# Performance work log

Measured on AMD Instinct MI355X. Metric: run time of the kernel, lower is better.

The kernel has to match this reference:

```python
import jax, jax.numpy as jnp
import numpy as np

B, N, D, H, DH, FF, CI, K, MPE = 8, 1024, 512, 8, 64, 2048, 1024, 31, 512
PAD = (K // 2, K // 2 - (K + 1) % 2)  # (15, 15)


def _ln(x, g, b):
    m = x.mean(-1, keepdims=True)
    v = ((x - m) ** 2).mean(-1, keepdims=True)
    return (x - m) * jax.lax.rsqrt(v + 1e-5) * g + b


def _swish(x):
    return x * jax.nn.sigmoid(x)


def setup_inputs() -> dict:
    key = jax.random.key(0)
    ks = iter(jax.random.split(key, 40))
    def w(shape, s=0.02):
        return (jax.random.normal(next(ks), shape) * s).astype(jnp.float32)
    ones = lambda n: jnp.ones((n,), jnp.float32)
    zeros = lambda n: jnp.zeros((n,), jnp.float32)
    return dict(
        x=jax.random.normal(next(ks), (B, N, D), dtype=jnp.float32),
        f1_g=ones(D), f1_b=zeros(D), f1_w1=w((D, FF)), f1_b1=zeros(FF), f1_w2=w((FF, D)), f1_b2=zeros(D),
        a_g=ones(D), a_b=zeros(D), wq=w((D, H * DH)), wkv=w((D, 2 * H * DH)), wo=w((H * DH, D)), wo_b=zeros(D),
        rel=w((2 * MPE + 1, DH)),
        c_g=ones(D), c_b=zeros(D), cw1=w((D, 2 * CI)), cb1=zeros(2 * CI), dw=w((CI, K)), db=zeros(CI),
        bn_g=ones(CI), bn_b=zeros(CI), bn_m=zeros(CI), bn_v=ones(CI), cw2=w((CI, D)), cb2=zeros(D),
        f2_g=ones(D), f2_b=zeros(D), f2_w1=w((D, FF)), f2_b1=zeros(FF), f2_w2=w((FF, D)), f2_b2=zeros(D),
        p_g=ones(D), p_b=zeros(D),
    )


def reference(x, f1_g, f1_b, f1_w1, f1_b1, f1_w2, f1_b2,
              a_g, a_b, wq, wkv, wo, wo_b, rel,
              c_g, c_b, cw1, cb1, dw, db, bn_g, bn_b, bn_m, bn_v, cw2, cb2,
              f2_g, f2_b, f2_w1, f2_b1, f2_w2, f2_b2, p_g, p_b):
    # FF1 (half-step)
    h = _ln(x, f1_g, f1_b)
    x = x + 0.5 * (_swish(h @ f1_w1 + f1_b1) @ f1_w2 + f1_b2)
    # Attention with relative positional bias
    h = _ln(x, a_g, a_b)
    q = (h @ wq).reshape(B, N, H, DH).transpose(0, 2, 1, 3)          # bhnd
    k, v = jnp.split(h @ wkv, 2, axis=-1)
    k = k.reshape(B, N, H, DH).transpose(0, 2, 1, 3)
    v = v.reshape(B, N, H, DH).transpose(0, 2, 1, 3)
    scale = DH ** -0.5
    dots = jnp.einsum('bhid,bhjd->bhij', q, k) * scale
    seq = jnp.arange(N)
    dist = jnp.clip(seq[:, None] - seq[None, :], -MPE, MPE) + MPE    # [N,N]
    rp = rel[dist]                                                   # [N,N,DH]
    dots = dots + jnp.einsum('bhnd,nrd->bhnr', q, rp) * scale
    attn = jax.nn.softmax(dots, axis=-1)
    o = jnp.einsum('bhij,bhjd->bhid', attn, v).transpose(0, 2, 1, 3).reshape(B, N, H * DH)
    x = x + o @ wo + wo_b
    # Conv module: LN -> pw conv -> GLU -> depthwise conv -> BN(eval) -> swish -> pw conv
    h = _ln(x, c_g, c_b)
    h = h @ cw1 + cb1                                                # [B,N,2CI]
    out, gate = jnp.split(h, 2, axis=-1)
    h = (out * jax.nn.sigmoid(gate)).transpose(0, 2, 1)              # [B,CI,N]
    h = jnp.pad(h, ((0, 0), (0, 0), PAD))
    h = jax.lax.conv_general_dilated(h, dw[:, None, :], (1,), 'VALID',
                                     feature_group_count=CI,
                                     dimension_numbers=('NCH', 'OIH', 'NCH')) + db[None, :, None]
    h = (h - bn_m[None, :, None]) * jax.lax.rsqrt(bn_v[None, :, None] + 1e-5) * bn_g[None, :, None] + bn_b[None, :, None]
    h = _swish(h).transpose(0, 2, 1)                                 # [B,N,CI]
    x = x + h @ cw2 + cb2
    # FF2 (half-step) + post norm
    h = _ln(x, f2_g, f2_b)
    x = x + 0.5 * (_swish(h @ f2_w1 + f2_b1) @ f2_w2 + f2_b2)
    return _ln(x, p_g, p_b)
```

## Files before the change

kernel.cpp:

```cpp
#include <hip/hip_runtime.h>
#include <hip/hip_bf16.h>
#include <cstdint>


using bf16_t = __hip_bfloat16;
typedef __bf16 bf16x8 __attribute__((ext_vector_type(8)));
typedef float floatx4 __attribute__((ext_vector_type(4)));

struct alignas(16) hbf8 { bf16_t h[8]; };
struct alignas(8)  hbf4 { bf16_t h[4]; };

__device__ __forceinline__ float  b2f(bf16_t h) { return __bfloat162float(h); }
__device__ __forceinline__ bf16_t f2b(float f)  { return __float2bfloat16(f); }
__device__ __forceinline__ float  sig_(float x) { return 1.f / (1.f + __expf(-x)); }

__device__ __forceinline__ unsigned pkbf(float a, float b) {
  bf16_t ha = f2b(a), hb = f2b(b);
  unsigned short ua, ub;
  __builtin_memcpy(&ua, &ha, 2);
  __builtin_memcpy(&ub, &hb, 2);
  return (unsigned)ua | ((unsigned)ub << 16);
}

__device__ __forceinline__ void async16(const void* g, void* l) {
  __builtin_amdgcn_global_load_lds(
      (const __attribute__((address_space(1))) unsigned int*)(uintptr_t)g,
      (__attribute__((address_space(3))) unsigned int*)(uintptr_t)l, 16, 0, 0);
}

struct GemmArgs {
  const bf16_t* A; const bf16_t* Bt; const float* bias; const float* srcf;
  bf16_t* C; float* resid;
  int K, lda, ldb, ldc;
  long sAb, sAh, sBb, sBh, sCb, sCh;
  float alpha, beta;
};

template <int BM, int BN, int WR, int WC, int EPI>
__global__ __launch_bounds__(256) void gemm_bt(GemmArgs g) {
  constexpr int FM = BM / (WR * 16);
  constexpr int FN = BN / (WC * 16);
  constexpr int IA = BM / 32;
  constexpr int IB = BN / 32;
  __shared__ __align__(16) bf16_t As[BM * 64];
  __shared__ __align__(16) bf16_t Bs[BN * 64];
  const int tid = threadIdx.x;
  const int lane = tid & 63, w = tid >> 6;
  int bx = blockIdx.x, by = blockIdx.y;
  {
    const int gx = gridDim.x;
    const int nwg = gx * gridDim.y;
    if ((nwg & 7) == 0 && gridDim.z == 1) {
      int lin = by * gx + bx;
      int lid = (lin & 7) * (nwg >> 3) + (lin >> 3);
      bx = lid % gx; by = lid / gx;
    }
  }
  const int bm0 = by * BM, bn0 = bx * BN;
  const int zb = blockIdx.z >> 3, zh = blockIdx.z & 7;
  const bf16_t* Ab = g.A + (long)zb * g.sAb + (long)zh * g.sAh;
  const bf16_t* Bb = g.Bt + (long)zb * g.sBb + (long)zh * g.sBh;
  const int wm0 = (w / WC) * (FM * 16);
  const int wn0 = (w % WC) * (FN * 16);
  const int lrow = lane & 15, lq = lane >> 4;

  floatx4 acc[FM][FN] = {};

  for (int k0 = 0; k0 < g.K; k0 += 64) {
#pragma unroll
    for (int i = 0; i < IA; ++i) {
      int c = i * 256 + tid;
      int m = c >> 3, kk = (c & 7) * 8;
      async16(Ab + (long)(bm0 + m) * g.lda + (k0 + kk), (char*)As + c * 16);
    }
#pragma unroll
    for (int i = 0; i < IB; ++i) {
      int c = i * 256 + tid;
      int n = bn0 + (c >> 3), kk = (c & 7) * 8;
      async16(Bb + (long)n * g.ldb + (k0 + kk), (char*)Bs + c * 16);
    }
    __syncthreads();
#pragma unroll
    for (int ks = 0; ks < 2; ++ks) {
      bf16x8 af[FM], bfr[FN];
#pragma unroll
      for (int fm = 0; fm < FM; ++fm)
        af[fm] = *(const bf16x8*)(As + (wm0 + fm * 16 + lrow) * 64 + ks * 32 + lq * 8);
#pragma unroll
      for (int fn = 0; fn < FN; ++fn)
        bfr[fn] = *(const bf16x8*)(Bs + (wn0 + fn * 16 + lrow) * 64 + ks * 32 + lq * 8);
#pragma unroll
      for (int fm = 0; fm < FM; ++fm)
#pragma unroll
        for (int fn = 0; fn < FN; ++fn)
          acc[fm][fn] = __builtin_amdgcn_mfma_f32_16x16x32_bf16(af[fm], bfr[fn], acc[fm][fn], 0, 0, 0);
    }
    __syncthreads();
  }

  const int bi = bm0 + wm0 + lq * 4;
  const int bj = bn0 + wn0 + lrow;
  if constexpr (EPI == 2) {
    float* R = g.resid;
    const float* S = g.srcf;
#pragma unroll
    for (int fm = 0; fm < FM; ++fm)
#pragma unroll
      for (int fn = 0; fn < FN; ++fn) {
        int j = bj + fn * 16;
        float bv = g.bias ? g.bias[j] : 0.f;
#pragma unroll
        for (int r = 0; r < 4; ++r) {
          long i = bi + fm * 16 + r;
          float base = S ? S[i * g.ldc + j] : R[i * g.ldc + j];
          R[i * g.ldc + j] = base + g.beta * (acc[fm][fn][r] + bv);
        }
      }
  } else if constexpr (EPI == 4) {
    bf16_t* C = g.C;
#pragma unroll
    for (int fm = 0; fm < FM; ++fm)
#pragma unroll
      for (int fn = 0; fn < FN; ++fn) {
        int j = bj + fn * 16;
        float bv = g.bias[(j >> 1) + (j & 1) * 1024];
#pragma unroll
        for (int r = 0; r < 4; ++r) {
          int i = bi + fm * 16 + r;
          float v = acc[fm][fn][r] + bv;
          float gp = __shfl_xor(v, 1);
          if ((j & 1) == 0)
            C[(long)i * g.ldc + (j >> 1)] = f2b(v * sig_(gp));
        }
      }
  } else {
    bf16_t* C = g.C + (long)zb * g.sCb + (long)zh * g.sCh;
#pragma unroll
    for (int fm = 0; fm < FM; ++fm)
#pragma unroll
      for (int fn = 0; fn < FN; ++fn) {
        int j = bj + fn * 16;
        float bv = g.bias ? g.bias[j] : 0.f;
#pragma unroll
        for (int r = 0; r < 4; ++r) {
          int i = bi + fm * 16 + r;
          float v = acc[fm][fn][r];
          if constexpr (EPI == 0) v = g.alpha * v + bv;
          if constexpr (EPI == 1) { v += bv; v = v * sig_(v); }
          C[(long)i * g.ldc + j] = f2b(v);
        }
      }
  }
}

__global__ __launch_bounds__(512, 4) void attn_kernel(
    const bf16_t* __restrict__ QKV, const bf16_t* __restrict__ VT,
    const bf16_t* __restrict__ RELP, bf16_t* __restrict__ O) {
  constexpr int LDT = 1028;
  __shared__ __align__(16) bf16_t Tls[32 * LDT];
  __shared__ float scr[576];

  const int tid = threadIdx.x;
  const int w = tid >> 6, lane = tid & 63;
  const int lrow = lane & 15, lq = lane >> 4;
  const int lin = blockIdx.y * gridDim.x + blockIdx.x;
  const int lid = (lin & 7) * 256 + (lin >> 3);
  const int z = lid >> 5;
  const int i0 = (lid & 31) * 32;
  const int b = z >> 3, zh = z & 7;
  const int j0w = w * 128;

  const bf16_t* Qb  = QKV + ((long)(b * 1024 + i0)) * 1536 + zh * 64;
  const bf16_t* Kb  = QKV + ((long)b * 1024) * 1536 + 512 + zh * 64;
  const bf16_t* VTb = VT + ((long)(b * 8 + zh)) * 65536;

  bf16x8 af[2][2];
#pragma unroll
  for (int fm = 0; fm < 2; ++fm)
#pragma unroll
    for (int ks = 0; ks < 2; ++ks)
      af[fm][ks] = *(const bf16x8*)(Qb + (long)(fm * 16 + lrow) * 1536 + ks * 32 + lq * 8);

  {
    const int u0w = w * 144;
    bf16x8 rf[18];
#pragma unroll
    for (int fnT = 0; fnT < 9; ++fnT) {
      const int u0 = u0w + fnT * 16;
      if (u0 <= 1024) {
        rf[2 * fnT]     = *(const bf16x8*)(RELP + (long)(u0 + lrow) * 64 + lq * 8);
        rf[2 * fnT + 1] = *(const bf16x8*)(RELP + (long)(u0 + lrow) * 64 + 32 + lq * 8);
      }
    }
#pragma unroll
    for (int fnT = 0; fnT < 9; ++fnT) {
      const int u0 = u0w + fnT * 16;
      if (u0 <= 1024) {
#pragma unroll
        for (int fm = 0; fm < 2; ++fm) {
          floatx4 t4 = {};
          t4 = __builtin_amdgcn_mfma_f32_16x16x32_bf16(rf[2 * fnT],     af[fm][0], t4, 0, 0, 0);
          t4 = __builtin_amdgcn_mfma_f32_16x16x32_bf16(rf[2 * fnT + 1], af[fm][1], t4, 0, 0, 0);
          if (u0 + lq * 4 + 4 <= LDT) {
            uint2 v; v.x = pkbf(t4[0], t4[1]); v.y = pkbf(t4[2], t4[3]);
            *(uint2*)(Tls + (long)(fm * 16 + lrow) * LDT + u0 + lq * 4) = v;
          }
        }
      }
    }
  }

  bf16x8 kfA[8], kfB[8];
#pragma unroll
  for (int x = 0; x < 8; ++x)
    kfA[x] = *(const bf16x8*)(Kb + (long)(j0w + (x >> 1) * 16 + lrow) * 1536 + (x & 1) * 32 + lq * 8);
#pragma unroll
  for (int x = 0; x < 8; ++x)
    kfB[x] = *(const bf16x8*)(Kb + (long)(j0w + (4 + (x >> 1)) * 16 + lrow) * 1536 + (x & 1) * 32 + lq * 8);
  __syncthreads();

  floatx4 sacc[2][8] = {};
#pragma unroll
  for (int fn = 0; fn < 4; ++fn) {
    sacc[0][fn] = __builtin_amdgcn_mfma_f32_16x16x32_bf16(af[0][0], kfA[2 * fn],     sacc[0][fn], 0, 0, 0);
    sacc[0][fn] = __builtin_amdgcn_mfma_f32_16x16x32_bf16(af[0][1], kfA[2 * fn + 1], sacc[0][fn], 0, 0, 0);
    sacc[1][fn] = __builtin_amdgcn_mfma_f32_16x16x32_bf16(af[1][0], kfA[2 * fn],     sacc[1][fn], 0, 0, 0);
    sacc[1][fn] = __builtin_amdgcn_mfma_f32_16x16x32_bf16(af[1][1], kfA[2 * fn + 1], sacc[1][fn], 0, 0, 0);
  }
#pragma unroll
  for (int fn = 4; fn < 8; ++fn) {
    sacc[0][fn] = __builtin_amdgcn_mfma_f32_16x16x32_bf16(af[0][0], kfB[2 * (fn - 4)],     sacc[0][fn], 0, 0, 0);
    sacc[0][fn] = __builtin_amdgcn_mfma_f32_16x16x32_bf16(af[0][1], kfB[2 * (fn - 4) + 1], sacc[0][fn], 0, 0, 0);
    sacc[1][fn] = __builtin_amdgcn_mfma_f32_16x16x32_bf16(af[1][0], kfB[2 * (fn - 4)],     sacc[1][fn], 0, 0, 0);
    sacc[1][fn] = __builtin_amdgcn_mfma_f32_16x16x32_bf16(af[1][1], kfB[2 * (fn - 4) + 1], sacc[1][fn], 0, 0, 0);
  }

#pragma unroll
  for (int fm = 0; fm < 2; ++fm)
#pragma unroll
    for (int r = 0; r < 4; ++r) {
      const int il = fm * 16 + lq * 4 + r;
      const bf16_t* trow = Tls + il * LDT + 512;
      const int tb = i0 + il - j0w - lrow;
#pragma unroll
      for (int fn = 0; fn < 8; ++fn) {
        int t = tb - fn * 16;
        t = t < -512 ? -512 : (t > 512 ? 512 : t);
        sacc[fm][fn][r] += b2f(trow[t]);
      }
    }

  float rmax[2][4];
#pragma unroll
  for (int fm = 0; fm < 2; ++fm)
#pragma unroll
    for (int r = 0; r < 4; ++r) {
      float m = sacc[fm][0][r];
#pragma unroll
      for (int fn = 1; fn < 8; ++fn) m = fmaxf(m, sacc[fm][fn][r]);
      rmax[fm][r] = m;
    }
#pragma unroll
  for (int off = 1; off < 16; off <<= 1)
#pragma unroll
    for (int fm = 0; fm < 2; ++fm)
#pragma unroll
      for (int r = 0; r < 4; ++r)
        rmax[fm][r] = fmaxf(rmax[fm][r], __shfl_xor(rmax[fm][r], off));
  if (lrow == 0)
#pragma unroll
    for (int fm = 0; fm < 2; ++fm)
#pragma unroll
      for (int r = 0; r < 4; ++r)
        scr[(fm * 16 + lq * 4 + r) * 9 + w] = rmax[fm][r];

  float rsum[2][4];
#pragma unroll
  for (int fm = 0; fm < 2; ++fm)
#pragma unroll
    for (int r = 0; r < 4; ++r) {
      float s = 0.f;
#pragma unroll
      for (int fn = 0; fn < 8; ++fn) {
        float e = __expf(sacc[fm][fn][r] - rmax[fm][r]);
        sacc[fm][fn][r] = e;
        s += e;
      }
      rsum[fm][r] = s;
    }
#pragma unroll
  for (int off = 1; off < 16; off <<= 1)
#pragma unroll
    for (int fm = 0; fm < 2; ++fm)
#pragma unroll
      for (int r = 0; r < 4; ++r)
        rsum[fm][r] += __shfl_xor(rsum[fm][r], off);
  if (lrow == 0)
#pragma unroll
    for (int fm = 0; fm < 2; ++fm)
#pragma unroll
      for (int r = 0; r < 4; ++r)
        scr[288 + (fm * 16 + lq * 4 + r) * 9 + w] = rsum[fm][r];

  bf16x8 vfA[8];
#pragma unroll
  for (int x = 0; x < 8; ++x)
    vfA[x] = *(const bf16x8*)(VTb + (long)((x & 3) * 16 + lrow) * 1024 + j0w + (x >> 2) * 32 + lq * 8);

  __syncthreads();

#pragma unroll
  for (int fm = 0; fm < 2; ++fm)
#pragma unroll
    for (int fn = 0; fn < 8; ++fn)
#pragma unroll
      for (int r = 0; r < 4; ++r) {
        const int i = fm * 16 + lq * 4 + r;
        const int j = j0w + fn * 16 + lrow;
        const unsigned boff = (unsigned)(i * 2048 + j * 2) ^ ((unsigned)(i & 7) << 4);
        *(bf16_t*)((char*)Tls + boff) = f2b(sacc[fm][fn][r]);
      }

  bf16x8 vfB[8];
#pragma unroll
  for (int x = 0; x < 8; ++x)
    vfB[x] = *(const bf16x8*)(VTb + (long)((x & 3) * 16 + lrow) * 1024 + j0w + 64 + (x >> 2) * 32 + lq * 8);

  floatx4 oacc[2][4] = {};
#pragma unroll
  for (int ks = 0; ks < 4; ++ks) {
    const int j = j0w + ks * 32;
    bf16x8 ap[2];
#pragma unroll
    for (int fm = 0; fm < 2; ++fm) {
      const int i = fm * 16 + lrow;
      const unsigned boff = (unsigned)(i * 2048 + (j + lq * 8) * 2) ^ ((unsigned)(i & 7) << 4);
      ap[fm] = *(const bf16x8*)((char*)Tls + boff);
    }
#pragma unroll
    for (int fd = 0; fd < 4; ++fd) {
      bf16x8 bv = (ks < 2) ? vfA[(ks << 2) | fd] : vfB[((ks - 2) << 2) | fd];
      oacc[0][fd] = __builtin_amdgcn_mfma_f32_16x16x32_bf16(ap[0], bv, oacc[0][fd], 0, 0, 0);
      oacc[1][fd] = __builtin_amdgcn_mfma_f32_16x16x32_bf16(ap[1], bv, oacc[1][fd], 0, 0, 0);
    }
  }
  __syncthreads();

  {
    float* part = (float*)Tls + w * 2048;
#pragma unroll
    for (int fm = 0; fm < 2; ++fm)
#pragma unroll
      for (int fd = 0; fd < 4; ++fd)
#pragma unroll
        for (int r = 0; r < 4; ++r)
          part[(fm * 16 + lq * 4 + r) * 64 + fd * 16 + lrow] = oacc[fm][fd][r];
  }
  __syncthreads();

  {
    const int i = tid >> 4;
    const int d0 = (tid & 15) * 4;
    float mw[8], sw[8];
#pragma unroll
    for (int ww = 0; ww < 8; ++ww) {
      mw[ww] = scr[i * 9 + ww];
      sw[ww] = scr[288 + i * 9 + ww];
    }
    float M = mw[0];
#pragma unroll
    for (int ww = 1; ww < 8; ++ww) M = fmaxf(M, mw[ww]);
    float fac[8]; float tot = 0.f;
#pragma unroll
    for (int ww = 0; ww < 8; ++ww) { fac[ww] = __expf(mw[ww] - M); tot += sw[ww] * fac[ww]; }
    const float inv = 1.f / tot;
    floatx4 s = {};
#pragma unroll
    for (int ww = 0; ww < 8; ++ww) {
      floatx4 p = *(const floatx4*)((const float*)Tls + ww * 2048 + i * 64 + d0);
      s += p * fac[ww];
    }
    hbf4 o4;
#pragma unroll
    for (int m = 0; m < 4; ++m) o4.h[m] = f2b(s[m] * inv);
    *(hbf4*)(O + (long)(b * 1024 + i0 + i) * 512 + zh * 64 + d0) = o4;
  }
}

__global__ __launch_bounds__(256) void diag_kernel(float* __restrict__ out, long n, float v) {
  long i = (long)blockIdx.x * 256 + threadIdx.x;
  if (i < n) out[i] = v;
}

struct PrepJobs {
  const float* src[10];
  bf16_t*      dst[10];
  int R[10], C[10], gx[10], start[10];
  float scale[10];
  int   mode[10];
  int   njobs;
};

__global__ __launch_bounds__(256) void prep_kernel(PrepJobs P) {
  __shared__ float t[32][33];
  const int bid = blockIdx.x;
  int j = 0;
  while (j + 1 < P.njobs && bid >= P.start[j + 1]) ++j;
  const int tile = bid - P.start[j];
  const int tid = threadIdx.x;
  if (P.mode[j] == 2) {
    int i = tile * 256 + tid;
    if (i < 73728) {
      int r = i >> 6, c = i & 63;
      P.dst[j][i] = (r < 1025) ? f2b(P.src[j][r * 64 + c]) : f2b(0.f);
    }
    return;
  }
  const int gx = P.gx[j];
  const int c0 = (tile % gx) * 32, r0 = (tile / gx) * 32;
  const int C = P.C[j], R = P.R[j];
  const float scale = P.scale[j];
  const int tx = tid & 31, ty = tid >> 5;
#pragma unroll
  for (int i = 0; i < 4; ++i)
    t[ty + i * 8][tx] = P.src[j][(long)(r0 + ty + i * 8) * C + c0 + tx];
  __syncthreads();
#pragma unroll
  for (int i = 0; i < 4; ++i) {
    int c = c0 + ty + i * 8;
    int row = (P.mode[j] == 1) ? ((c < 1024) ? 2 * c : 2 * (c - 1024) + 1) : c;
    P.dst[j][(long)row * R + r0 + tx] = f2b(t[tx][ty + i * 8] * scale);
  }
}

template <bool F32OUT>
__global__ __launch_bounds__(256) void ln_kernel(const float* __restrict__ X, const float* __restrict__ gam,
                                                 const float* __restrict__ bet, void* __restrict__ outv) {
  int row = blockIdx.x, tid = threadIdx.x;
  const float* x = X + (long)row * 512;
  float a = x[tid], b = x[tid + 256];
  float s = a + b, q = a * a + b * b;
  for (int off = 32; off; off >>= 1) { s += __shfl_down(s, off); q += __shfl_down(q, off); }
  __shared__ float red[8];
  int w = tid >> 6;
  if ((tid & 63) == 0) { red[w] = s; red[w + 4] = q; }
  __syncthreads();
  float ts = red[0] + red[1] + red[2] + red[3];
  float tq = red[4] + red[5] + red[6] + red[7];
  float mean = ts * (1.f / 512.f);
  float var = tq * (1.f / 512.f) - mean * mean;
  float rs = rsqrtf(var + 1e-5f);
  float o0 = (a - mean) * rs * gam[tid]       + bet[tid];
  float o1 = (b - mean) * rs * gam[tid + 256] + bet[tid + 256];
  if constexpr (F32OUT) {
    float* out = (float*)outv;
    out[(long)row * 512 + tid]       = o0;
    out[(long)row * 512 + tid + 256] = o1;
  } else {
    bf16_t* out = (bf16_t*)outv;
    out[(long)row * 512 + tid]       = f2b(o0);
    out[(long)row * 512 + tid + 256] = f2b(o1);
  }
}

__global__ __launch_bounds__(256) void vt_kernel(const bf16_t* __restrict__ QKV, bf16_t* __restrict__ VT) {
  int jb = blockIdx.x, z = blockIdx.y;
  int b = z >> 3, h = z & 7;
  const bf16_t* src = QKV + (long)b * 1024 * 1536 + 1024 + h * 64;
  bf16_t* dst = VT + (long)z * 65536;
  __shared__ bf16_t t[64][65];
  int tid = threadIdx.x;
#pragma unroll
  for (int i = 0; i < 16; ++i) {
    int l = i * 256 + tid;
    int j = l >> 6, d = l & 63;
    t[d][j] = src[(long)(jb * 64 + j) * 1536 + d];
  }
  __syncthreads();
#pragma unroll
  for (int i = 0; i < 16; ++i) {
    int l = i * 256 + tid;
    int d = l >> 6, j = l & 63;
    dst[(long)d * 1024 + jb * 64 + j] = t[d][j];
  }
}

__global__ __launch_bounds__(256) void dwconv_kernel(const bf16_t* __restrict__ G, const float* __restrict__ dw,
    const float* __restrict__ db, const float* __restrict__ bng, const float* __restrict__ bnb,
    const float* __restrict__ bnm, const float* __restrict__ bnv, bf16_t* __restrict__ out) {
  int n0 = blockIdx.x * 32, c0 = blockIdx.y * 64, b = blockIdx.z;
  __shared__ bf16_t t[62][64];
  __shared__ float dws[31][64];
  int tid = threadIdx.x;
  const bf16_t* src = G + (long)b * 1024 * 1024 + c0;
#pragma unroll
  for (int i = 0; i < 2; ++i) {
    int l = i * 256 + tid;
    if (l < 496) {
      int rr = l >> 3, c8 = (l & 7) * 8;
      int n = n0 - 15 + rr;
      hbf8 v;
      if (n >= 0 && n < 1024) v = *(const hbf8*)(src + (long)n * 1024 + c8);
      else { for (int m = 0; m < 8; ++m) v.h[m] = f2b(0.f); }
      *(hbf8*)&t[rr][c8] = v;
    }
  }
#pragma unroll
  for (int i = 0; i < 8; ++i) {
    int l = i * 256 + tid;
    if (l < 1984) {
      int k = l >> 6, c = l & 63;
      dws[k][c] = dw[(long)(c0 + c) * 31 + k];
    }
  }
  __syncthreads();
  int c = tid & 63, nl = tid >> 6;
  float rs = rsqrtf(bnv[c0 + c] + 1e-5f);
  float sc = rs * bng[c0 + c];
  float ab = (db[c0 + c] - bnm[c0 + c]) * sc + bnb[c0 + c];
#pragma unroll
  for (int j = 0; j < 8; ++j) {
    int rr = nl * 8 + j;
    float s = 0.f;
#pragma unroll
    for (int k = 0; k < 31; ++k) s += b2f(t[rr + k][c]) * dws[k][c];
    float y = s * sc + ab;
    out[((long)b * 1024 + n0 + rr) * 1024 + c0 + c] = f2b(y * sig_(y));
  }
}

extern "C" void kernel_launch(void* const* d_in, const int* in_sizes, int n_in,
                              void* d_out, int out_size, void* d_ws, size_t ws_size,
                              hipStream_t stream) {
  auto fail = [&](float code) {
    diag_kernel<<<(out_size + 255) / 256, 256, 0, stream>>>((float*)d_out, out_size, code);
  };
  if (n_in != 34)             { fail(70.f);  return; }
  if (in_sizes[0] != 4194304) { fail(80.f);  return; }

  const float* x     = (const float*)d_in[0];
  const float* f1_g  = (const float*)d_in[1];
  const float* f1_b  = (const float*)d_in[2];
  const float* f1_w1 = (const float*)d_in[3];
  const float* f1_b1 = (const float*)d_in[4];
  const float* f1_w2 = (const float*)d_in[5];
  const float* f1_b2 = (const float*)d_in[6];
  const float* a_g   = (const float*)d_in[7];
  const float* a_b   = (const float*)d_in[8];
  const float* wq    = (const float*)d_in[9];
  const float* wkv   = (const float*)d_in[10];
  const float* wo    = (const float*)d_in[11];
  const float* wo_b  = (const float*)d_in[12];
  const float* rel   = (const float*)d_in[13];
  const float* c_g   = (const float*)d_in[14];
  const float* c_b   = (const float*)d_in[15];
  const float* cw1   = (const float*)d_in[16];
  const float* cb1   = (const float*)d_in[17];
  const float* dwp   = (const float*)d_in[18];
  const float* dbp   = (const float*)d_in[19];
  const float* bn_g  = (const float*)d_in[20];
  const float* bn_b  = (const float*)d_in[21];
  const float* bn_m  = (const float*)d_in[22];
  const float* bn_v  = (const float*)d_in[23];
  const float* cw2   = (const float*)d_in[24];
  const float* cb2   = (const float*)d_in[25];
  const float* f2_g  = (const float*)d_in[26];
  const float* f2_b  = (const float*)d_in[27];
  const float* f2_w1 = (const float*)d_in[28];
  const float* f2_b1 = (const float*)d_in[29];
  const float* f2_w2 = (const float*)d_in[30];
  const float* f2_b2 = (const float*)d_in[31];
  const float* p_g   = (const float*)d_in[32];
  const float* p_b   = (const float*)d_in[33];

  char* ws = (char*)d_ws;
  const size_t OFF_X  = 0;
  const size_t OFF_WT = 16777216;
  const size_t OFF_D  = 30408704;
  const size_t OFF_E  = 63963136;
  const size_t relp_off = OFF_E + 33554432;
  if (ws_size < relp_off + 147456ULL) { fail(200.f); return; }

  float*  X   = (float*)(ws + OFF_X);
  bf16_t* WT  = (bf16_t*)(ws + OFF_WT);
  bf16_t* QKV = (bf16_t*)(ws + OFF_D);
  bf16_t* VT  = (bf16_t*)(ws + OFF_D + 25165824);
  bf16_t* GLU = (bf16_t*)(ws + OFF_D);
  bf16_t* DWO = (bf16_t*)(ws + OFF_D + 16777216);
  bf16_t* MID = (bf16_t*)(ws + OFF_E);
  bf16_t* RELP= (bf16_t*)(ws + relp_off);
  bf16_t* H   = (bf16_t*)d_out;
  bf16_t* O   = (bf16_t*)d_out;

  bf16_t* f1_w1t = WT;            bf16_t* f1_w2t = WT + 1048576;
  bf16_t* wqkvt  = WT + 2097152;
  bf16_t* wot    = WT + 2883584;  bf16_t* cw1t   = WT + 3145728;
  bf16_t* cw2t   = WT + 4194304;  bf16_t* f2_w1t = WT + 4718592;
  bf16_t* f2_w2t = WT + 5767168;

  auto GA = [](const bf16_t* A, const bf16_t* Bt, const float* bias, bf16_t* C,
               float* resid, const float* srcf, int K, int lda, int ldb, int ldc,
               float alpha, float beta) {
    GemmArgs g{}; g.A = A; g.Bt = Bt; g.bias = bias; g.srcf = srcf; g.C = C; g.resid = resid;
    g.K = K; g.lda = lda; g.ldb = ldb; g.ldc = ldc;
    g.sAb = g.sAh = g.sBb = g.sBh = g.sCb = g.sCh = 0; g.alpha = alpha; g.beta = beta;
    return g;
  };

  {
    PrepJobs P{};
    auto set = [&](int idx, const float* s, bf16_t* d, int R, int C, int start,
                   float sc, int mode) {
      P.src[idx] = s; P.dst[idx] = d; P.R[idx] = R; P.C[idx] = C;
      P.gx[idx] = C / 32; P.start[idx] = start; P.scale[idx] = sc; P.mode[idx] = mode;
    };
    set(0, f1_w1, f1_w1t,          512, 2048,    0, 1.f,    0);
    set(1, f1_w2, f1_w2t,         2048,  512, 1024, 1.f,    0);
    set(2, wq,    wqkvt,           512,  512, 2048, 0.125f, 0);
    set(3, wkv,   wqkvt + 262144,  512, 1024, 2304, 1.f,    0);
    set(4, wo,    wot,             512,  512, 2816, 1.f,    0);
    set(5, cw1,   cw1t,            512, 2048, 3072, 1.f,    1);
    set(6, cw2,   cw2t,           1024,  512, 4096, 1.f,    0);
    set(7, f2_w1, f2_w1t,          512, 2048, 4608, 1.f,    0);
    set(8, f2_w2, f2_w2t,         2048,  512, 5632, 1.f,    0);
    set(9, rel,   RELP,           1025,   64, 6656, 1.f,    2);
    P.njobs = 10;
    prep_kernel<<<6944, 256, 0, stream>>>(P);
  }

  ln_kernel<false><<<8192, 256, 0, stream>>>(x, f1_g, f1_b, H);
  { GemmArgs g = GA(H, f1_w1t, f1_b1, MID, nullptr, nullptr, 512, 512, 512, 2048, 1.f, 0.f);
    gemm_bt<128, 128, 2, 2, 1><<<dim3(16, 64, 1), 256, 0, stream>>>(g); }
  { GemmArgs g = GA(MID, f1_w2t, f1_b2, nullptr, X, x, 2048, 2048, 2048, 512, 1.f, 0.5f);
    gemm_bt<64, 128, 1, 4, 2><<<dim3(4, 128, 1), 256, 0, stream>>>(g); }

  ln_kernel<false><<<8192, 256, 0, stream>>>(X, a_g, a_b, H);
  { GemmArgs g = GA(H, wqkvt, nullptr, QKV, nullptr, nullptr, 512, 512, 512, 1536, 1.f, 0.f);
    gemm_bt<128, 128, 2, 2, 0><<<dim3(12, 64, 1), 256, 0, stream>>>(g); }
  vt_kernel<<<dim3(16, 64), 256, 0, stream>>>(QKV, VT);

  attn_kernel<<<dim3(32, 64), 512, 0, stream>>>(QKV, VT, RELP, O);

  { GemmArgs g = GA(O, wot, wo_b, nullptr, X, nullptr, 512, 512, 512, 512, 1.f, 1.f);
    gemm_bt<64, 128, 1, 4, 2><<<dim3(4, 128, 1), 256, 0, stream>>>(g); }

  ln_kernel<false><<<8192, 256, 0, stream>>>(X, c_g, c_b, H);
  { GemmArgs g = GA(H, cw1t, cb1, GLU, nullptr, nullptr, 512, 512, 512, 1024, 1.f, 0.f);
    gemm_bt<128, 128, 2, 2, 4><<<dim3(16, 64, 1), 256, 0, stream>>>(g); }
  dwconv_kernel<<<dim3(32, 16, 8), 256, 0, stream>>>(GLU, dwp, dbp, bn_g, bn_b, bn_m, bn_v, DWO);
  { GemmArgs g = GA(DWO, cw2t, cb2, nullptr, X, nullptr, 1024, 1024, 1024, 512, 1.f, 1.f);
    gemm_bt<64, 128, 1, 4, 2><<<dim3(4, 128, 1), 256, 0, stream>>>(g); }

  ln_kernel<false><<<8192, 256, 0, stream>>>(X, f2_g, f2_b, H);
  { GemmArgs g = GA(H, f2_w1t, f2_b1, MID, nullptr, nullptr, 512, 512, 512, 2048, 1.f, 0.f);
    gemm_bt<128, 128, 2, 2, 1><<<dim3(16, 64, 1), 256, 0, stream>>>(g); }
  { GemmArgs g = GA(MID, f2_w2t, f2_b2, nullptr, X, nullptr, 2048, 2048, 2048, 512, 1.f, 0.5f);
    gemm_bt<64, 128, 1, 4, 2><<<dim3(4, 128, 1), 256, 0, stream>>>(g); }
  ln_kernel<true><<<8192, 256, 0, stream>>>(X, p_g, p_b, (float*)d_out);
}
```

Measured before the change: 632.3 us.

## Fuse V transpose into QKV GEMM epilogue and halve GEMM K-tile

```diff
diff --git a/kernel.cpp b/kernel.cpp
--- a/kernel.cpp
+++ b/kernel.cpp
@@ -30,7 +30,7 @@
 
 struct GemmArgs {
   const bf16_t* A; const bf16_t* Bt; const float* bias; const float* srcf;
-  bf16_t* C; float* resid;
+  bf16_t* C; bf16_t* C2; float* resid;
   int K, lda, ldb, ldc;
   long sAb, sAh, sBb, sBh, sCb, sCh;
   float alpha, beta;
@@ -40,10 +40,10 @@
 __global__ __launch_bounds__(256) void gemm_bt(GemmArgs g) {
   constexpr int FM = BM / (WR * 16);
   constexpr int FN = BN / (WC * 16);
-  constexpr int IA = BM / 32;
-  constexpr int IB = BN / 32;
-  __shared__ __align__(16) bf16_t As[BM * 64];
-  __shared__ __align__(16) bf16_t Bs[BN * 64];
+  constexpr int IA = (BM * 4) / 256;
+  constexpr int IB = (BN * 4) / 256;
+  __shared__ __align__(16) bf16_t As[BM * 32];
+  __shared__ __align__(16) bf16_t Bs[BN * 32];
   const int tid = threadIdx.x;
   const int lane = tid & 63, w = tid >> 6;
   int bx = blockIdx.x, by = blockIdx.y;
@@ -66,35 +66,32 @@
 
   floatx4 acc[FM][FN] = {};
 
-  for (int k0 = 0; k0 < g.K; k0 += 64) {
+  for (int k0 = 0; k0 < g.K; k0 += 32) {
 #pragma unroll
     for (int i = 0; i < IA; ++i) {
       int c = i * 256 + tid;
-      int m = c >> 3, kk = (c & 7) * 8;
+      int m = c >> 2, kk = (c & 3) * 8;
       async16(Ab + (long)(bm0 + m) * g.lda + (k0 + kk), (char*)As + c * 16);
     }
 #pragma unroll
     for (int i = 0; i < IB; ++i) {
       int c = i * 256 + tid;
-      int n = bn0 + (c >> 3), kk = (c & 7) * 8;
+      int n = bn0 + (c >> 2), kk = (c & 3) * 8;
       async16(Bb + (long)n * g.ldb + (k0 + kk), (char*)Bs + c * 16);
     }
     __syncthreads();
-#pragma unroll
-    for (int ks = 0; ks < 2; ++ks) {
-      bf16x8 af[FM], bfr[FN];
-#pragma unroll
-      for (int fm = 0; fm < FM; ++fm)
-        af[fm] = *(const bf16x8*)(As + (wm0 + fm * 16 + lrow) * 64 + ks * 32 + lq * 8);
+    bf16x8 af[FM], bfr[FN];
+#pragma unroll
+    for (int fm = 0; fm < FM; ++fm)
+      af[fm] = *(const bf16x8*)(As + (wm0 + fm * 16 + lrow) * 32 + lq * 8);
+#pragma unroll
+    for (int fn = 0; fn < FN; ++fn)
+      bfr[fn] = *(const bf16x8*)(Bs + (wn0 + fn * 16 + lrow) * 32 + lq * 8);
+#pragma unroll
+    for (int fm = 0; fm < FM; ++fm)
 #pragma unroll
       for (int fn = 0; fn < FN; ++fn)
-        bfr[fn] = *(const bf16x8*)(Bs + (wn0 + fn * 16 + lrow) * 64 + ks * 32 + lq * 8);
-#pragma unroll
-      for (int fm = 0; fm < FM; ++fm)
-#pragma unroll
-        for (int fn = 0; fn < FN; ++fn)
-          acc[fm][fn] = __builtin_amdgcn_mfma_f32_16x16x32_bf16(af[fm], bfr[fn], acc[fm][fn], 0, 0, 0);
-    }
+        acc[fm][fn] = __builtin_amdgcn_mfma_f32_16x16x32_bf16(af[fm], bfr[fn], acc[fm][fn], 0, 0, 0);
     __syncthreads();
   }
 
@@ -131,6 +128,31 @@
           float gp = __shfl_xor(v, 1);
           if ((j & 1) == 0)
             C[(long)i * g.ldc + (j >> 1)] = f2b(v * sig_(gp));
+        }
+      }
+  } else if constexpr (EPI == 5) {
+    bf16_t* C = g.C;
+    bf16_t* VTo = g.C2;
+#pragma unroll
+    for (int fm = 0; fm < FM; ++fm)
+#pragma unroll
+      for (int fn = 0; fn < FN; ++fn) {
+        int j = bj + fn * 16;
+        if (j < 1024) {
+#pragma unroll
+          for (int r = 0; r < 4; ++r) {
+            int i = bi + fm * 16 + r;
+            C[(long)i * g.ldc + j] = f2b(acc[fm][fn][r]);
+          }
+        } else {
+          int vc = j - 1024;
+          int h = vc >> 6, d = vc & 63;
+          int ib = bi + fm * 16;
+          int bb = ib >> 10, n = ib & 1023;
+          hbf4 o4;
+#pragma unroll
+          for (int r = 0; r < 4; ++r) o4.h[r] = f2b(acc[fm][fn][r]);
+          *(hbf4*)(VTo + (long)(bb * 8 + h) * 65536 + (long)d * 1024 + n) = o4;
         }
       }
   } else {
@@ -460,28 +482,6 @@
     bf16_t* out = (bf16_t*)outv;
     out[(long)row * 512 + tid]       = f2b(o0);
     out[(long)row * 512 + tid + 256] = f2b(o1);
-  }
-}
-
-__global__ __launch_bounds__(256) void vt_kernel(const bf16_t* __restrict__ QKV, bf16_t* __restrict__ VT) {
-  int jb = blockIdx.x, z = blockIdx.y;
-  int b = z >> 3, h = z & 7;
-  const bf16_t* src = QKV + (long)b * 1024 * 1536 + 1024 + h * 64;
-  bf16_t* dst = VT + (long)z * 65536;
-  __shared__ bf16_t t[64][65];
-  int tid = threadIdx.x;
-#pragma unroll
-  for (int i = 0; i < 16; ++i) {
-    int l = i * 256 + tid;
-    int j = l >> 6, d = l & 63;
-    t[d][j] = src[(long)(jb * 64 + j) * 1536 + d];
-  }
-  __syncthreads();
-#pragma unroll
-  for (int i = 0; i < 16; ++i) {
-    int l = i * 256 + tid;
-    int d = l >> 6, j = l & 63;
-    dst[(long)d * 1024 + jb * 64 + j] = t[d][j];
   }
 }
 
@@ -601,7 +601,8 @@
   auto GA = [](const bf16_t* A, const bf16_t* Bt, const float* bias, bf16_t* C,
                float* resid, const float* srcf, int K, int lda, int ldb, int ldc,
                float alpha, float beta) {
-    GemmArgs g{}; g.A = A; g.Bt = Bt; g.bias = bias; g.srcf = srcf; g.C = C; g.resid = resid;
+    GemmArgs g{}; g.A = A; g.Bt = Bt; g.bias = bias; g.srcf = srcf; g.C = C; g.C2 = nullptr;
+    g.resid = resid;
     g.K = K; g.lda = lda; g.ldb = ldb; g.ldc = ldc;
     g.sAb = g.sAh = g.sBb = g.sBh = g.sCb = g.sCh = 0; g.alpha = alpha; g.beta = beta;
     return g;
@@ -636,8 +637,8 @@
 
   ln_kernel<false><<<8192, 256, 0, stream>>>(X, a_g, a_b, H);
   { GemmArgs g = GA(H, wqkvt, nullptr, QKV, nullptr, nullptr, 512, 512, 512, 1536, 1.f, 0.f);
-    gemm_bt<128, 128, 2, 2, 0><<<dim3(12, 64, 1), 256, 0, stream>>>(g); }
-  vt_kernel<<<dim3(16, 64), 256, 0, stream>>>(QKV, VT);
+    g.C2 = VT;
+    gemm_bt<128, 128, 2, 2, 5><<<dim3(12, 64, 1), 256, 0, stream>>>(g); }
 
   attn_kernel<<<dim3(32, 64), 512, 0, stream>>>(QKV, VT, RELP, O);
 
```

Result: no change. 625.6 us (-1.1%).
